# Kernel optimization log

Measured on AMD Instinct MI355X. Metric: run time of the kernel, lower is better.

Reference implementation:

```python
import jax, jax.numpy as jnp
import numpy as np

T = 131072
INPUT_DIM = 256
OUTPUT_DIM = 8
BN_EPS = 1e-3  # keras BatchNormalization default epsilon


def setup_inputs() -> dict:
    key = jax.random.key(0)
    ks = jax.random.split(key, 9)
    d_in = INPUT_DIM + OUTPUT_DIM
    s1 = np.sqrt(1.0 / INPUT_DIM)
    s2 = np.sqrt(1.0 / 64)
    s3 = np.sqrt(1.0 / 32)
    return {
        "x": jax.random.normal(ks[0], (T, INPUT_DIM), dtype=jnp.float32),
        "gamma": jnp.ones((INPUT_DIM,), jnp.float32),
        "beta": jnp.zeros((INPUT_DIM,), jnp.float32),
        "W1": jax.random.uniform(ks[1], (d_in, 64), jnp.float32, -s1, s1),
        "b1": jnp.zeros((64,), jnp.float32),
        "W2": jax.random.uniform(ks[2], (64, 32), jnp.float32, -s2, s2),
        "b2": jnp.zeros((32,), jnp.float32),
        "W3": jax.random.uniform(ks[3], (32, OUTPUT_DIM), jnp.float32, -s3, s3),
        "b3": jnp.zeros((OUTPUT_DIM,), jnp.float32),
    }


def reference(x, gamma, beta, W1, b1, W2, b2, W3, b3):
    # BatchNorm (training mode): batch statistics over the leading axis
    mean = jnp.mean(x, axis=0)
    var = jnp.var(x, axis=0)  # biased variance, as in keras BN
    xn = gamma * (x - mean) * jax.lax.rsqrt(var + BN_EPS) + beta

    # Sequential loop with output fed back as state (RNN-like)
    def step(h, xi):
        z = jnp.concatenate([xi, h])            # [input_dim + output_dim]
        h1 = jax.nn.relu(z @ W1 + b1)           # [64]
        h2 = jax.nn.relu(h1 @ W2 + b2)          # [32]
        o = h2 @ W3 + b3                        # [output_dim]
        return o, o

    h0 = jnp.zeros((W3.shape[1],), x.dtype)
    _, out = jax.lax.scan(step, h0, xn)
    return out  # [T, output_dim]
```

## Files before the change

kernel.cpp:

```cpp
#include <hip/hip_runtime.h>
#include <hip/hip_bf16.h>

typedef unsigned short u16;
typedef unsigned int   u32;
typedef __attribute__((ext_vector_type(8))) short short8;
typedef __attribute__((ext_vector_type(4))) float f32x4;

#define T_ROWS   131072
#define L_CHUNK  16
#define WARM     8
#define NCHUNK   (T_ROWS / L_CHUNK)

#define WS_SUM   0
#define WS_SQ    256
#define WS_CJ    512
#define WS_WEF   576
#define WS_PRE_BYTES ((size_t)(WS_WEF + 8192) * 4)
#define WS_NEED  (WS_PRE_BYTES + (size_t)T_ROWS * 64 * 2)

__device__ __forceinline__ u16 f2bf(float f) {
  u32 u = __float_as_uint(f);
  u += 0x7FFFu + ((u >> 16) & 1u);
  return (u16)(u >> 16);
}

template <int CTRL>
__device__ __forceinline__ float dpp_take(float v) {
  return __int_as_float(
      __builtin_amdgcn_update_dpp(0, __float_as_int(v), CTRL, 0xF, 0xF, true));
}
__device__ __forceinline__ float swz_xor16(float v) {
  return __int_as_float(__builtin_amdgcn_ds_swizzle(__float_as_int(v), 0x401F));
}

__global__ void k_zero(float* ws) { ws[threadIdx.x] = 0.0f; }

__global__ void k_sentinel(float* out) { out[threadIdx.x] = 12345.0f; }

__global__ __launch_bounds__(256) void k_stats(const float* __restrict__ x,
                                               float* __restrict__ ws) {
  __shared__ float lsum[1024];
  __shared__ float lsq[1024];
  const int tid = threadIdx.x;
  const int lane = tid & 63;
  const int w = tid >> 6;
  const int c = lane * 4;
  float s0 = 0, s1 = 0, s2 = 0, s3 = 0;
  float q0 = 0, q1 = 0, q2 = 0, q3 = 0;
  const size_t rbase = (size_t)blockIdx.x * 128;
  for (int i = w; i < 128; i += 4) {
    const float4 v = *(const float4*)(x + (rbase + i) * 256 + c);
    s0 += v.x; s1 += v.y; s2 += v.z; s3 += v.w;
    q0 = fmaf(v.x, v.x, q0); q1 = fmaf(v.y, v.y, q1);
    q2 = fmaf(v.z, v.z, q2); q3 = fmaf(v.w, v.w, q3);
  }
  lsum[w * 256 + c + 0] = s0; lsum[w * 256 + c + 1] = s1;
  lsum[w * 256 + c + 2] = s2; lsum[w * 256 + c + 3] = s3;
  lsq [w * 256 + c + 0] = q0; lsq [w * 256 + c + 1] = q1;
  lsq [w * 256 + c + 2] = q2; lsq [w * 256 + c + 3] = q3;
  __syncthreads();
  const float ts = lsum[tid] + lsum[256 + tid] + lsum[512 + tid] + lsum[768 + tid];
  const float tq = lsq [tid] + lsq [256 + tid] + lsq [512 + tid] + lsq [768 + tid];
  atomicAdd(ws + WS_SUM + tid, ts);
  atomicAdd(ws + WS_SQ  + tid, tq);
}

__global__ __launch_bounds__(256) void k_prep(const float* __restrict__ gamma,
                                              const float* __restrict__ beta,
                                              const float* __restrict__ W1,
                                              const float* __restrict__ b1,
                                              float* __restrict__ ws) {
  __shared__ float sScale[256];
  __shared__ float sShift[256];
  __shared__ float sCj[256];
  const int tid = threadIdx.x;
  const float inv = 1.0f / (float)T_ROWS;
  const float mean = ws[WS_SUM + tid] * inv;
  const float var  = ws[WS_SQ + tid] * inv - mean * mean;
  const float sc = gamma[tid] * rsqrtf(var + 1e-3f);
  const float sh = beta[tid] - mean * sc;
  sScale[tid] = sc;
  sShift[tid] = sh;
  __syncthreads();
  const int nt = tid >> 6;
  const int lane = tid & 63;
  const int m = lane & 15;
  const int q = lane >> 4;
  const int n = nt * 16 + m;
  u32* Wf = (u32*)(ws + WS_WEF);
#pragma unroll
  for (int ks = 0; ks < 8; ++ks) {
    uint4 pk;
    u32 w_[4];
#pragma unroll
    for (int jj = 0; jj < 4; ++jj) {
      const int k0 = ks * 32 + q * 8 + 2 * jj;
      const u32 lo = f2bf(sScale[k0]     * W1[(size_t)k0 * 64 + n]);
      const u32 hi = f2bf(sScale[k0 + 1] * W1[(size_t)(k0 + 1) * 64 + n]);
      w_[jj] = lo | (hi << 16);
    }
    pk.x = w_[0]; pk.y = w_[1]; pk.z = w_[2]; pk.w = w_[3];
    *(uint4*)(Wf + (size_t)((ks * 4 + nt) * 64 + lane) * 4) = pk;
  }
  const int j = tid & 63;
  const int part = tid >> 6;
  float p = (part == 0) ? b1[j] : 0.0f;
  for (int c = part * 64; c < part * 64 + 64; ++c)
    p = fmaf(sShift[c], W1[(size_t)c * 64 + j], p);
  sCj[tid] = p;
  __syncthreads();
  if (tid < 64)
    ws[WS_CJ + tid] = sCj[tid] + sCj[64 + tid] + sCj[128 + tid] + sCj[192 + tid];
}

__global__ __launch_bounds__(256) void k_gemm(const float* __restrict__ x,
                                              const float* __restrict__ ws,
                                              u16* __restrict__ pre1t) {
  const int lane = threadIdx.x & 63;
  const int w = threadIdx.x >> 6;
  const int m = lane & 15;
  const int q = lane >> 4;
  const size_t r0 = (size_t)blockIdx.x * 64 + (size_t)w * 16;
  const size_t p = r0 >> 4;
  const float* xr = x + (r0 + m) * 256 + q * 8;
  const u32* Bf = (const u32*)(ws + WS_WEF);

  f32x4 acc[4];
#pragma unroll
  for (int nt = 0; nt < 4; ++nt) acc[nt] = (f32x4){0.f, 0.f, 0.f, 0.f};

#pragma unroll
  for (int ks = 0; ks < 8; ++ks) {
    const float4 xa = *(const float4*)(xr + ks * 32);
    const float4 xb = *(const float4*)(xr + ks * 32 + 4);
    union { short8 v; u32 u[4]; } A;
    A.u[0] = f2bf(xa.x) | ((u32)f2bf(xa.y) << 16);
    A.u[1] = f2bf(xa.z) | ((u32)f2bf(xa.w) << 16);
    A.u[2] = f2bf(xb.x) | ((u32)f2bf(xb.y) << 16);
    A.u[3] = f2bf(xb.z) | ((u32)f2bf(xb.w) << 16);
#pragma unroll
    for (int nt = 0; nt < 4; ++nt) {
      const short8 Bv = *(const short8*)(Bf + (size_t)((ks * 4 + nt) * 64 + lane) * 4);
      acc[nt] = __builtin_amdgcn_mfma_f32_16x16x32_bf16(A.v, Bv, acc[nt], 0, 0, 0);
    }
  }
#pragma unroll
  for (int nt = 0; nt < 4; ++nt) {
    const float c = ws[WS_CJ + nt * 16 + m];
    uint2 pk;
    pk.x = (u32)f2bf(acc[nt][0] + c) | ((u32)f2bf(acc[nt][1] + c) << 16);
    pk.y = (u32)f2bf(acc[nt][2] + c) | ((u32)f2bf(acc[nt][3] + c) << 16);
    *(uint2*)(pre1t + p * 1024 + (size_t)(nt * 16 + m) * 16 + q * 4) = pk;
  }
}

__global__ __launch_bounds__(256, 4) void k_scan(const u16* __restrict__ pre1t,
                                                 const float* __restrict__ W1,
                                                 const float* __restrict__ W2,
                                                 const float* __restrict__ b2,
                                                 const float* __restrict__ W3,
                                                 const float* __restrict__ b3,
                                                 float* __restrict__ out) {
  const int tid = threadIdx.x;
  const int lane = tid & 63;
  const int wv = tid >> 6;
  const int p = blockIdx.x * 4 + wv;
  const int m = lane & 31;
  const int half = lane >> 5;
  const int outStart = p * L_CHUNK;

  float Wh[8];
#pragma unroll
  for (int k = 0; k < 8; ++k) Wh[k] = W1[(256 + k) * 64 + lane];
  float W2r[32];
#pragma unroll
  for (int i = 0; i < 32; ++i) W2r[i] = W2[(32 * half + i) * 32 + m];
  const float b2r = b2[m];
  float W3r[8], b3r[8];
#pragma unroll
  for (int n = 0; n < 8; ++n) W3r[n] = W3[m * 8 + n];
#pragma unroll
  for (int n = 0; n < 8; ++n) b3r[n] = b3[n];

  __shared__ __align__(16) float lh1[4][64];

  const u16* base = pre1t + (size_t)p * 1024 + (size_t)lane * 16;
  const uint4 mv0 = *(const uint4*)(base);
  const uint4 mv1 = *(const uint4*)(base + 8);
  uint4 wv4 = make_uint4(0, 0, 0, 0);
  if (p > 0) wv4 = *(const uint4*)(base - 1024 + 8);
  const u32 preW[4] = {wv4.x, wv4.y, wv4.z, wv4.w};
  const u32 preM[8] = {mv0.x, mv0.y, mv0.z, mv0.w, mv1.x, mv1.y, mv1.z, mv1.w};

  float h[8];
#pragma unroll
  for (int n = 0; n < 8; ++n) h[n] = 0.0f;
  float osv[8];
#pragma unroll
  for (int n = 0; n < 8; ++n) osv[n] = 0.0f;

  auto step = [&](float pf, bool save, int slane) {
    float a0 = pf, a1 = 0.0f;
#pragma unroll
    for (int k = 0; k < 4; ++k) {
      a0 = fmaf(h[2 * k],     Wh[2 * k],     a0);
      a1 = fmaf(h[2 * k + 1], Wh[2 * k + 1], a1);
    }
    const float h1 = fmaxf(a0 + a1, 0.0f);
    __builtin_amdgcn_wave_barrier();
    lh1[wv][lane] = h1;
    __builtin_amdgcn_wave_barrier();
    const float4* qv = (const float4*)(lh1[wv] + half * 32);
    float c0 = 0, c1 = 0, c2 = 0, c3 = 0;
#pragma unroll
    for (int r = 0; r < 8; ++r) {
      const float4 v = qv[r];
      c0 = fmaf(v.x, W2r[4 * r + 0], c0);
      c1 = fmaf(v.y, W2r[4 * r + 1], c1);
      c2 = fmaf(v.z, W2r[4 * r + 2], c2);
      c3 = fmaf(v.w, W2r[4 * r + 3], c3);
    }
    const float part = (c0 + c1) + (c2 + c3);
    const float h2 = fmaxf(part + __shfl_xor(part, 32, 64) + b2r, 0.0f);
    float o[8];
#pragma unroll
    for (int n = 0; n < 8; ++n) o[n] = h2 * W3r[n];
#pragma unroll
    for (int n = 0; n < 8; ++n) o[n] += dpp_take<0xB1>(o[n]);
#pragma unroll
    for (int n = 0; n < 8; ++n) o[n] += dpp_take<0x4E>(o[n]);
#pragma unroll
    for (int n = 0; n < 8; ++n) o[n] += dpp_take<0x141>(o[n]);
#pragma unroll
    for (int n = 0; n < 8; ++n) o[n] += dpp_take<0x140>(o[n]);
#pragma unroll
    for (int n = 0; n < 8; ++n) o[n] += swz_xor16(o[n]);
#pragma unroll
    for (int n = 0; n < 8; ++n) h[n] = o[n] + b3r[n];
    if (save) {
      const bool mine = (lane == slane);
#pragma unroll
      for (int n = 0; n < 8; ++n) osv[n] = mine ? h[n] : osv[n];
    }
  };

  if (p > 0) {
#pragma unroll
    for (int i = 0; i < 8; ++i) {
      const u32 wd = preW[i >> 1];
      const float pf = (i & 1) ? __uint_as_float(wd & 0xFFFF0000u)
                               : __uint_as_float(wd << 16);
      step(pf, false, -1);
    }
  }
#pragma unroll
  for (int u = 0; u < 16; ++u) {
    const u32 wd = preM[u >> 1];
    const float pf = (u & 1) ? __uint_as_float(wd & 0xFFFF0000u)
                             : __uint_as_float(wd << 16);
    step(pf, true, u);
  }

  if (lane < 16) {
    float4* dst = (float4*)(out + (size_t)(outStart + lane) * 8);
    dst[0] = make_float4(osv[0], osv[1], osv[2], osv[3]);
    dst[1] = make_float4(osv[4], osv[5], osv[6], osv[7]);
  }
}

extern "C" void kernel_launch(void* const* d_in, const int* in_sizes, int n_in,
                              void* d_out, int out_size, void* d_ws, size_t ws_size,
                              hipStream_t stream) {
  (void)in_sizes; (void)n_in; (void)out_size;
  const float* x     = (const float*)d_in[0];
  const float* gamma = (const float*)d_in[1];
  const float* beta  = (const float*)d_in[2];
  const float* W1    = (const float*)d_in[3];
  const float* b1    = (const float*)d_in[4];
  const float* W2    = (const float*)d_in[5];
  const float* b2    = (const float*)d_in[6];
  const float* W3    = (const float*)d_in[7];
  const float* b3    = (const float*)d_in[8];
  float* out = (float*)d_out;
  float* ws  = (float*)d_ws;
  u16* pre1t = (u16*)((char*)d_ws + WS_PRE_BYTES);

  if (ws_size < WS_NEED) {
    k_sentinel<<<1, 64, 0, stream>>>(out);
    return;
  }
  k_zero <<<1,    512, 0, stream>>>(ws);
  k_stats<<<1024, 256, 0, stream>>>(x, ws);
  k_prep <<<1,    256, 0, stream>>>(gamma, beta, W1, b1, ws);
  k_gemm <<<2048, 256, 0, stream>>>(x, ws, pre1t);
  k_scan <<<NCHUNK / 4, 256, 0, stream>>>(pre1t, W1, W2, b2, W3, b3, out);
}
```

Measured before the change: 307.3 us.

## Double scan chunk length to cut warm-up overhead and relayout pre-activations

Raises the per-wave scan chunk from 16 to 32 timesteps, so the fixed 8-step warm-up recompute is amortised over more outputs. The k_gemm output layout changes to 32-step chunks to match, and the scan now loads pre-activations with a software-prefetched loop of 4 steps at a time instead of preloading everything. k_prep is widened to 512 threads and k_stats gets an unroll hint. The trade-offs are half as many scan waves, each with a longer serial dependency chain, which may lower parallelism, and a loop that is no longer fully unrolled.

Result: faster. 292.8 us (-4.7%).

```diff
diff --git a/kernel.cpp b/kernel.cpp
--- a/kernel.cpp
+++ b/kernel.cpp
@@ -7,7 +7,7 @@
 typedef __attribute__((ext_vector_type(4))) float f32x4;
 
 #define T_ROWS   131072
-#define L_CHUNK  16
+#define L_CHUNK  32
 #define WARM     8
 #define NCHUNK   (T_ROWS / L_CHUNK)
 
@@ -48,6 +48,7 @@
   float s0 = 0, s1 = 0, s2 = 0, s3 = 0;
   float q0 = 0, q1 = 0, q2 = 0, q3 = 0;
   const size_t rbase = (size_t)blockIdx.x * 128;
+#pragma unroll 4
   for (int i = w; i < 128; i += 4) {
     const float4 v = *(const float4*)(x + (rbase + i) * 256 + c);
     s0 += v.x; s1 += v.y; s2 += v.z; s3 += v.w;
@@ -65,52 +66,59 @@
   atomicAdd(ws + WS_SQ  + tid, tq);
 }
 
-__global__ __launch_bounds__(256) void k_prep(const float* __restrict__ gamma,
+__global__ __launch_bounds__(512) void k_prep(const float* __restrict__ gamma,
                                               const float* __restrict__ beta,
                                               const float* __restrict__ W1,
                                               const float* __restrict__ b1,
                                               float* __restrict__ ws) {
   __shared__ float sScale[256];
   __shared__ float sShift[256];
-  __shared__ float sCj[256];
+  __shared__ float sCj[512];
   const int tid = threadIdx.x;
-  const float inv = 1.0f / (float)T_ROWS;
-  const float mean = ws[WS_SUM + tid] * inv;
-  const float var  = ws[WS_SQ + tid] * inv - mean * mean;
-  const float sc = gamma[tid] * rsqrtf(var + 1e-3f);
-  const float sh = beta[tid] - mean * sc;
-  sScale[tid] = sc;
-  sShift[tid] = sh;
+  if (tid < 256) {
+    const float inv = 1.0f / (float)T_ROWS;
+    const float mean = ws[WS_SUM + tid] * inv;
+    const float var  = ws[WS_SQ + tid] * inv - mean * mean;
+    const float sc = gamma[tid] * rsqrtf(var + 1e-3f);
+    sScale[tid] = sc;
+    sShift[tid] = beta[tid] - mean * sc;
+  }
   __syncthreads();
-  const int nt = tid >> 6;
-  const int lane = tid & 63;
-  const int m = lane & 15;
-  const int q = lane >> 4;
-  const int n = nt * 16 + m;
-  u32* Wf = (u32*)(ws + WS_WEF);
-#pragma unroll
-  for (int ks = 0; ks < 8; ++ks) {
-    uint4 pk;
-    u32 w_[4];
-#pragma unroll
-    for (int jj = 0; jj < 4; ++jj) {
-      const int k0 = ks * 32 + q * 8 + 2 * jj;
-      const u32 lo = f2bf(sScale[k0]     * W1[(size_t)k0 * 64 + n]);
-      const u32 hi = f2bf(sScale[k0 + 1] * W1[(size_t)(k0 + 1) * 64 + n]);
-      w_[jj] = lo | (hi << 16);
-    }
-    pk.x = w_[0]; pk.y = w_[1]; pk.z = w_[2]; pk.w = w_[3];
-    *(uint4*)(Wf + (size_t)((ks * 4 + nt) * 64 + lane) * 4) = pk;
+  if (tid < 256) {
+    const int nt = tid >> 6;
+    const int lane = tid & 63;
+    const int m = lane & 15;
+    const int q = lane >> 4;
+    const int n = nt * 16 + m;
+    u32* Wf = (u32*)(ws + WS_WEF);
+#pragma unroll
+    for (int ks = 0; ks < 8; ++ks) {
+      uint4 pk;
+      u32 w_[4];
+#pragma unroll
+      for (int jj = 0; jj < 4; ++jj) {
+        const int k0 = ks * 32 + q * 8 + 2 * jj;
+        const u32 lo = f2bf(sScale[k0]     * W1[(size_t)k0 * 64 + n]);
+        const u32 hi = f2bf(sScale[k0 + 1] * W1[(size_t)(k0 + 1) * 64 + n]);
+        w_[jj] = lo | (hi << 16);
+      }
+      pk.x = w_[0]; pk.y = w_[1]; pk.z = w_[2]; pk.w = w_[3];
+      *(uint4*)(Wf + (size_t)((ks * 4 + nt) * 64 + lane) * 4) = pk;
+    }
   }
   const int j = tid & 63;
   const int part = tid >> 6;
   float p = (part == 0) ? b1[j] : 0.0f;
-  for (int c = part * 64; c < part * 64 + 64; ++c)
+  for (int c = part * 32; c < part * 32 + 32; ++c)
     p = fmaf(sShift[c], W1[(size_t)c * 64 + j], p);
   sCj[tid] = p;
   __syncthreads();
-  if (tid < 64)
-    ws[WS_CJ + tid] = sCj[tid] + sCj[64 + tid] + sCj[128 + tid] + sCj[192 + tid];
+  if (tid < 64) {
+    float a = 0.0f;
+#pragma unroll
+    for (int k = 0; k < 8; ++k) a += sCj[k * 64 + tid];
+    ws[WS_CJ + tid] = a;
+  }
 }
 
 __global__ __launch_bounds__(256) void k_gemm(const float* __restrict__ x,
@@ -121,7 +129,8 @@
   const int m = lane & 15;
   const int q = lane >> 4;
   const size_t r0 = (size_t)blockIdx.x * 64 + (size_t)w * 16;
-  const size_t p = r0 >> 4;
+  const size_t p = r0 >> 5;
+  const int tbase = ((int)r0 & 16) + q * 4;
   const float* xr = x + (r0 + m) * 256 + q * 8;
   const u32* Bf = (const u32*)(ws + WS_WEF);
 
@@ -150,7 +159,7 @@
     uint2 pk;
     pk.x = (u32)f2bf(acc[nt][0] + c) | ((u32)f2bf(acc[nt][1] + c) << 16);
     pk.y = (u32)f2bf(acc[nt][2] + c) | ((u32)f2bf(acc[nt][3] + c) << 16);
-    *(uint2*)(pre1t + p * 1024 + (size_t)(nt * 16 + m) * 16 + q * 4) = pk;
+    *(uint2*)(pre1t + p * 2048 + (size_t)(nt * 16 + m) * 32 + tbase) = pk;
   }
 }
 
@@ -184,22 +193,13 @@
 
   __shared__ __align__(16) float lh1[4][64];
 
-  const u16* base = pre1t + (size_t)p * 1024 + (size_t)lane * 16;
-  const uint4 mv0 = *(const uint4*)(base);
-  const uint4 mv1 = *(const uint4*)(base + 8);
-  uint4 wv4 = make_uint4(0, 0, 0, 0);
-  if (p > 0) wv4 = *(const uint4*)(base - 1024 + 8);
-  const u32 preW[4] = {wv4.x, wv4.y, wv4.z, wv4.w};
-  const u32 preM[8] = {mv0.x, mv0.y, mv0.z, mv0.w, mv1.x, mv1.y, mv1.z, mv1.w};
-
-  float h[8];
-#pragma unroll
-  for (int n = 0; n < 8; ++n) h[n] = 0.0f;
-  float osv[8];
-#pragma unroll
-  for (int n = 0; n < 8; ++n) osv[n] = 0.0f;
-
-  auto step = [&](float pf, bool save, int slane) {
+  const u16* base2 = pre1t + (size_t)p * 2048 + (size_t)lane * 32;
+
+  float h[8], osv[8];
+#pragma unroll
+  for (int n = 0; n < 8; ++n) { h[n] = 0.0f; osv[n] = 0.0f; }
+
+  auto step = [&](float pf, int rel) {
     float a0 = pf, a1 = 0.0f;
 #pragma unroll
     for (int k = 0; k < 4; ++k) {
@@ -237,31 +237,30 @@
     for (int n = 0; n < 8; ++n) o[n] += swz_xor16(o[n]);
 #pragma unroll
     for (int n = 0; n < 8; ++n) h[n] = o[n] + b3r[n];
-    if (save) {
-      const bool mine = (lane == slane);
-#pragma unroll
-      for (int n = 0; n < 8; ++n) osv[n] = mine ? h[n] : osv[n];
-    }
+    const bool mine = (lane == rel);
+#pragma unroll
+    for (int n = 0; n < 8; ++n) osv[n] = mine ? h[n] : osv[n];
   };
 
-  if (p > 0) {
-#pragma unroll
-    for (int i = 0; i < 8; ++i) {
-      const u32 wd = preW[i >> 1];
-      const float pf = (i & 1) ? __uint_as_float(wd & 0xFFFF0000u)
-                               : __uint_as_float(wd << 16);
-      step(pf, false, -1);
-    }
-  }
-#pragma unroll
-  for (int u = 0; u < 16; ++u) {
-    const u32 wd = preM[u >> 1];
-    const float pf = (u & 1) ? __uint_as_float(wd & 0xFFFF0000u)
-                             : __uint_as_float(wd << 16);
-    step(pf, true, u);
-  }
-
-  if (lane < 16) {
+  auto ldpf = [&](int rel) -> uint2 {
+    return *(const uint2*)(base2 + rel + ((rel < 0) ? -2016 : 0));
+  };
+
+  int t = (p > 0) ? -WARM : 0;
+  uint2 cur = ldpf(t);
+  for (; t < L_CHUNK; t += 4) {
+    int tn = t + 4;
+    if (tn > L_CHUNK - 4) tn = L_CHUNK - 4;
+    const uint2 nxt = ldpf(tn);
+    const u32 w0 = cur.x, w1 = cur.y;
+    step(__uint_as_float(w0 << 16),          t);
+    step(__uint_as_float(w0 & 0xFFFF0000u),  t + 1);
+    step(__uint_as_float(w1 << 16),          t + 2);
+    step(__uint_as_float(w1 & 0xFFFF0000u),  t + 3);
+    cur = nxt;
+  }
+
+  if (lane < 32) {
     float4* dst = (float4*)(out + (size_t)(outStart + lane) * 8);
     dst[0] = make_float4(osv[0], osv[1], osv[2], osv[3]);
     dst[1] = make_float4(osv[4], osv[5], osv[6], osv[7]);
@@ -291,7 +290,7 @@
   }
   k_zero <<<1,    512, 0, stream>>>(ws);
   k_stats<<<1024, 256, 0, stream>>>(x, ws);
-  k_prep <<<1,    256, 0, stream>>>(gamma, beta, W1, b1, ws);
+  k_prep <<<1,    512, 0, stream>>>(gamma, beta, W1, b1, ws);
   k_gemm <<<2048, 256, 0, stream>>>(x, ws, pre1t);
   k_scan <<<NCHUNK / 4, 256, 0, stream>>>(pre1t, W1, W2, b2, W3, b3, out);
 }
```
